# Kernel tuning notes

Hardware: AMD Instinct MI355X
Metric: run time of the kernel (lower is better)

Reference implementation:

```python
import jax, jax.numpy as jnp
import numpy as np

N_NODES = 20000
N_EDGES = 40000
N_GRAPHS = 500
D_IN = 32     # initial_dim_gcn
D_E = 16      # edge_dim_feature
H1 = 100      # hidden_dim_nn_1
H2 = 20       # hidden_dim_nn_2
F1 = 50       # hidden_dim_fcn_1


def setup_inputs() -> dict:
    key = jax.random.key(0)
    ks = jax.random.split(key, 16)
    s = lambda k, shp, fan: (jax.random.normal(k, shp, jnp.float32) / np.sqrt(fan)).astype(jnp.float32)
    return {
        "x": jax.random.normal(ks[0], (N_NODES, D_IN), jnp.float32),
        "edge_attr": jax.random.normal(ks[1], (N_EDGES, D_E), jnp.float32),
        "edge_index": jax.random.randint(ks[2], (2, N_EDGES), 0, N_NODES, jnp.int64),
        "batch": jnp.sort(jax.random.randint(ks[3], (N_NODES,), 0, N_GRAPHS, jnp.int64)),
        # NNConv layer 1: edge MLP Linear(D_E -> D_IN*H1), root weight, bias
        "nn1_W": s(ks[4], (D_E, D_IN * H1), D_E),
        "nn1_b": jnp.zeros((D_IN * H1,), jnp.float32),
        "root1": s(ks[5], (D_IN, H1), D_IN),
        "bias1": jnp.zeros((H1,), jnp.float32),
        # NNConv layer 2: edge MLP Linear(D_E -> H1*H2), root weight, bias
        "nn2_W": s(ks[6], (D_E, H1 * H2), D_E),
        "nn2_b": jnp.zeros((H1 * H2,), jnp.float32),
        "root2": s(ks[7], (H1, H2), H1),
        "bias2": jnp.zeros((H2,), jnp.float32),
        # FCN head
        "lin1_W": s(ks[8], (H2, F1), H2),
        "lin1_b": jnp.zeros((F1,), jnp.float32),
        "lin2_W": s(ks[9], (F1, 1), F1),
        "lin2_b": jnp.zeros((1,), jnp.float32),
    }


def _nnconv(x, src, dst, edge_attr, nnW, nnb, root, bias, d_in, d_out):
    # per-edge weight matrices: [E, d_in, d_out]
    theta = (edge_attr @ nnW + nnb).reshape(-1, d_in, d_out)
    # gather source features, per-edge matmul, scatter-add to targets
    msg = jnp.einsum('ei,eio->eo', x[src], theta)            # [E, d_out]
    agg = jax.ops.segment_sum(msg, dst, num_segments=x.shape[0])
    return agg + x @ root + bias


def reference(x, edge_attr, edge_index, batch,
              nn1_W, nn1_b, root1, bias1,
              nn2_W, nn2_b, root2, bias2,
              lin1_W, lin1_b, lin2_W, lin2_b):
    src, dst = edge_index[0], edge_index[1]  # PyG: message from j=src, aggregate at i=dst
    h = jax.nn.relu(_nnconv(x, src, dst, edge_attr, nn1_W, nn1_b, root1, bias1, D_IN, H1))
    h = jax.nn.relu(_nnconv(h, src, dst, edge_attr, nn2_W, nn2_b, root2, bias2, H1, H2))
    g = jax.ops.segment_sum(h, batch, num_segments=N_GRAPHS)  # sum-pool readout [G, H2]
    g = jax.nn.relu(g @ lin1_W + lin1_b)
    out = g @ lin2_W + lin2_b
    return out.reshape(-1)
```

## Files before the change

### kernel.cpp

```cpp
#include <hip/hip_runtime.h>
#include <hip/hip_fp16.h>

#define N_NODES 20000
#define N_EDGES 40000
#define N_GRAPHS 500
#define D_IN 32
#define D_E 16
#define H1 100
#define H2 20
#define F1 50

#define EB1 64
#define YNB 12
#define ET3 12

using h2f = __attribute__((ext_vector_type(2))) _Float16;
using h8f = __attribute__((ext_vector_type(8))) _Float16;
using f4  = __attribute__((ext_vector_type(4))) float;

__global__ __launch_bounds__(256) void prep_kernel(
    const float* __restrict__ nn1W, const float* __restrict__ nn1b,
    const float* __restrict__ nn2W, const float* __restrict__ nn2b,
    const float* __restrict__ root1, const float* __restrict__ bias1,
    const float* __restrict__ x,
    unsigned short* __restrict__ Wfrag1, unsigned short* __restrict__ Wfrag2,
    float* __restrict__ pre1, float* __restrict__ zbase)
{
  __shared__ float sroot1[D_IN * H1];
  __shared__ float sxl[YNB * D_IN];
  const int t   = threadIdx.x;
  const int tid = blockIdx.x * 256 + t;

  if (tid < 544 * 112) {
    const int c  = tid / 3584;
    const int r  = tid % 3584;
    const int to = r / 512;
    const int l  = (r % 512) >> 3;
    const int j  = r & 7;
    const int i  = (l >> 4) * 8 + j;
    const int o  = to * 16 + (l & 15);
    float v = 0.f;
    if (o < H1) v = (c < 16) ? nn1W[c * (D_IN * H1) + i * H1 + o] : nn1b[i * H1 + o];
    _Float16 hv = (_Float16)v;
    Wfrag1[tid] = __builtin_bit_cast(unsigned short, hv);
  } else if (tid < 544 * 112 + 17 * 4096) {
    const int t2 = tid - 544 * 112;
    const int c  = t2 >> 12;
    const int q  = (t2 >> 10) & 3;
    const int to = (t2 >> 9) & 1;
    const int l  = (t2 >> 3) & 63;
    const int j  = t2 & 7;
    const int i  = q * 32 + (l >> 4) * 8 + j;
    const int o  = to * 16 + (l & 15);
    float v = 0.f;
    if (i < H1 && o < H2)
      v = (c < 16) ? nn2W[c * (H1 * H2) + i * H2 + o] : nn2b[i * H2 + o];
    _Float16 hv = (_Float16)v;
    Wfrag2[t2] = __builtin_bit_cast(unsigned short, hv);
  }

  {
    float4* zp = (float4*)zbase;
    for (int i = tid; i < 102500; i += 512 * 256)
      zp[i] = make_float4(0.f, 0.f, 0.f, 0.f);
  }

  for (int idx = t; idx < 800; idx += 256)
    *(float4*)&sroot1[idx * 4] = *(const float4*)&root1[idx * 4];

  for (int tile = blockIdx.x; tile < 1667; tile += 512) {
    const int n0 = tile * YNB;
    __syncthreads();
    if (t < 96) {
      const int fo = t * 4;
      const int nn = fo >> 5;
      float4 v = make_float4(0.f, 0.f, 0.f, 0.f);
      if (n0 + nn < N_NODES) v = *(const float4*)&x[(size_t)n0 * D_IN + fo];
      *(float4*)&sxl[fo] = v;
    }
    __syncthreads();
    for (int idx = t; idx < YNB * H1; idx += 256) {
      const int nn = idx / H1, i = idx - nn * H1;
      const int n = n0 + nn;
      if (n < N_NODES) {
        float v = bias1[i];
        #pragma unroll 8
        for (int d = 0; d < D_IN; ++d)
          v = fmaf(sxl[nn * D_IN + d], sroot1[d * H1 + i], v);
        pre1[(size_t)n0 * H1 + idx] = v;
      }
    }
  }
}

__global__ __launch_bounds__(256, 3) void edge1_kernel(
    const float* __restrict__ x, const float* __restrict__ ea,
    const int* __restrict__ eidx, const unsigned short* __restrict__ Wfrag,
    float* __restrict__ agg1)
{
  __shared__ uint4 Plds[4 * 64];
  __shared__ uint4 Blds[2][7 * 64];
  __shared__ int   sdst[EB1];

  const int t    = threadIdx.x;
  const int lane = t & 63;
  const int w    = t >> 6;
  const int e0   = blockIdx.x * EB1;

  const int e_loc = t >> 2;
  const int jg    = t & 3;
  const int src   = eidx[e0 + e_loc];

  h2f xh[4];
  {
    const float4* xp = (const float4*)&x[(size_t)src * D_IN + jg * 8];
    float4 v0 = xp[0], v1 = xp[1];
    float xf[8] = {v0.x, v0.y, v0.z, v0.w, v1.x, v1.y, v1.z, v1.w};
    #pragma unroll
    for (int j = 0; j < 4; ++j) {
      h2f p; p[0] = (_Float16)xf[2*j]; p[1] = (_Float16)xf[2*j+1]; xh[j] = p;
    }
  }
  _Float16 eh[17];
  {
    const float4* ep = (const float4*)&ea[(size_t)(e0 + e_loc) * D_E];
    float4 v0 = ep[0], v1 = ep[1], v2 = ep[2], v3 = ep[3];
    float ef[16] = {v0.x,v0.y,v0.z,v0.w, v1.x,v1.y,v1.z,v1.w,
                    v2.x,v2.y,v2.z,v2.w, v3.x,v3.y,v3.z,v3.w};
    #pragma unroll
    for (int k = 0; k < 16; ++k) eh[k] = (_Float16)ef[k];
    eh[16] = (_Float16)1.0f;
  }
  if (t < EB1) sdst[t] = eidx[N_EDGES + e0 + t];

  const uint4* __restrict__ Bf = (const uint4*)Wfrag;
  {
    uint4 s0 = Bf[t];
    uint4 s1;
    if (t < 192) s1 = Bf[256 + t];
    Blds[0][t] = s0;
    if (t < 192) Blds[0][256 + t] = s1;
  }
  __syncthreads();

  f4 acc[7];
  #pragma unroll
  for (int to = 0; to < 7; ++to) acc[to] = f4{0.f, 0.f, 0.f, 0.f};

  const int pslot = w * 64 + (e_loc & 15) + 16 * jg;

  #pragma unroll
  for (int c = 0; c < 17; ++c) {
    uint4 s0, s1;
    if (c < 16) {
      const uint4* bn = Bf + (c + 1) * 448;
      s0 = bn[t];
      if (t < 192) s1 = bn[256 + t];
    }
    h2f es; es[0] = eh[c]; es[1] = eh[c];
    unsigned int pk[4];
    #pragma unroll
    for (int j = 0; j < 4; ++j) {
      h2f pr = xh[j] * es;
      pk[j] = __builtin_bit_cast(unsigned int, pr);
    }
    Plds[pslot] = make_uint4(pk[0], pk[1], pk[2], pk[3]);

    uint4 a = Plds[w * 64 + lane];
    h8f A = __builtin_bit_cast(h8f, a);

    const uint4* bb = &Blds[c & 1][0];
    #pragma unroll
    for (int to = 0; to < 7; ++to) {
      h8f B = __builtin_bit_cast(h8f, bb[to * 64 + lane]);
      acc[to] = __builtin_amdgcn_mfma_f32_16x16x32_f16(A, B, acc[to], 0, 0, 0);
    }
    if (c < 16) {
      Blds[(c + 1) & 1][t] = s0;
      if (t < 192) Blds[(c + 1) & 1][256 + t] = s1;
    }
    __syncthreads();
  }

  const int col = lane & 15, rowg = lane >> 4;
  #pragma unroll
  for (int r = 0; r < 4; ++r) {
    const int el = w * 16 + rowg * 4 + r;
    const int d = sdst[el];
    float* ap = agg1 + (size_t)d * H1;
    #pragma unroll
    for (int to = 0; to < 7; ++to) {
      const int o = to * 16 + col;
      if (o < H1) unsafeAtomicAdd(&ap[o], acc[to][r]);
    }
  }
}

__global__ __launch_bounds__(256, 3) void edge2m_kernel(
    const float* __restrict__ pre1, const float* __restrict__ ea,
    const int* __restrict__ eidx, const unsigned short* __restrict__ Wfrag2,
    float* __restrict__ agg2)
{
  __shared__ uint4 Plds[4][4][64];
  __shared__ uint4 Blds[2][512];
  __shared__ int   sdst[EB1];

  const int t    = threadIdx.x;
  const int lane = t & 63;
  const int w    = t >> 6;
  const int e0   = blockIdx.x * EB1;

  const int e_loc = t >> 2;
  const int jg    = t & 3;
  const int m     = e_loc & 15;
  const int src   = eidx[e0 + e_loc];

  h2f xh[16];
  {
    float xf[32];
    const float* hp = &pre1[(size_t)src * H1 + jg * 32];
    if (jg < 3) {
      #pragma unroll
      for (int q4 = 0; q4 < 8; ++q4) {
        float4 v = *(const float4*)&hp[q4 * 4];
        xf[q4*4+0] = fmaxf(v.x, 0.f); xf[q4*4+1] = fmaxf(v.y, 0.f);
        xf[q4*4+2] = fmaxf(v.z, 0.f); xf[q4*4+3] = fmaxf(v.w, 0.f);
      }
    } else {
      float4 v = *(const float4*)hp;
      xf[0] = fmaxf(v.x, 0.f); xf[1] = fmaxf(v.y, 0.f);
      xf[2] = fmaxf(v.z, 0.f); xf[3] = fmaxf(v.w, 0.f);
      #pragma unroll
      for (int ii = 4; ii < 32; ++ii) xf[ii] = 0.f;
    }
    #pragma unroll
    for (int j2 = 0; j2 < 16; ++j2) {
      h2f p; p[0] = (_Float16)xf[2*j2]; p[1] = (_Float16)xf[2*j2+1]; xh[j2] = p;
    }
  }
  _Float16 eh[17];
  {
    const float4* ep = (const float4*)&ea[(size_t)(e0 + e_loc) * D_E];
    float4 v0 = ep[0], v1 = ep[1], v2 = ep[2], v3 = ep[3];
    float ef[16] = {v0.x,v0.y,v0.z,v0.w, v1.x,v1.y,v1.z,v1.w,
                    v2.x,v2.y,v2.z,v2.w, v3.x,v3.y,v3.z,v3.w};
    #pragma unroll
    for (int k = 0; k < 16; ++k) eh[k] = (_Float16)ef[k];
    eh[16] = (_Float16)1.0f;
  }
  if (t < EB1) sdst[t] = eidx[N_EDGES + e0 + t];

  const uint4* __restrict__ Bf = (const uint4*)Wfrag2;
  {
    uint4 s0 = Bf[t];
    uint4 s1 = Bf[256 + t];
    Blds[0][t] = s0;
    Blds[0][256 + t] = s1;
  }
  {
    h2f es; es[0] = eh[0]; es[1] = eh[0];
    unsigned int pk[16];
    #pragma unroll
    for (int j2 = 0; j2 < 16; ++j2) {
      h2f pr = xh[j2] * es;
      pk[j2] = __builtin_bit_cast(unsigned int, pr);
    }
    #pragma unroll
    for (int oc = 0; oc < 4; ++oc)
      Plds[w][jg][16 * oc + m] = make_uint4(pk[4*oc], pk[4*oc+1], pk[4*oc+2], pk[4*oc+3]);
  }
  __syncthreads();

  f4 acc0 = f4{0.f, 0.f, 0.f, 0.f};
  f4 acc1 = f4{0.f, 0.f, 0.f, 0.f};

  #pragma unroll
  for (int c = 0; c < 17; ++c) {
    const int buf = c & 1;
    uint4 s0, s1;
    if (c < 16) {
      const uint4* bn = Bf + (c + 1) * 512;
      s0 = bn[t];
      s1 = bn[256 + t];
    }
    #pragma unroll
    for (int q = 0; q < 4; ++q) {
      uint4 a  = Plds[w][q][lane];
      uint4 b0 = Blds[buf][q * 128 + lane];
      uint4 b1 = Blds[buf][q * 128 + 64 + lane];
      h8f A  = __builtin_bit_cast(h8f, a);
      h8f B0 = __builtin_bit_cast(h8f, b0);
      h8f B1 = __builtin_bit_cast(h8f, b1);
      acc0 = __builtin_amdgcn_mfma_f32_16x16x32_f16(A, B0, acc0, 0, 0, 0);
      acc1 = __builtin_amdgcn_mfma_f32_16x16x32_f16(A, B1, acc1, 0, 0, 0);
    }
    if (c < 16) {
      h2f es; es[0] = eh[c + 1]; es[1] = eh[c + 1];
      unsigned int pk[16];
      #pragma unroll
      for (int j2 = 0; j2 < 16; ++j2) {
        h2f pr = xh[j2] * es;
        pk[j2] = __builtin_bit_cast(unsigned int, pr);
      }
      #pragma unroll
      for (int oc = 0; oc < 4; ++oc)
        Plds[w][jg][16 * oc + m] = make_uint4(pk[4*oc], pk[4*oc+1], pk[4*oc+2], pk[4*oc+3]);
      Blds[buf ^ 1][t] = s0;
      Blds[buf ^ 1][256 + t] = s1;
      __syncthreads();
    }
  }

  const int col = lane & 15, rowg = lane >> 4;
  #pragma unroll
  for (int r = 0; r < 4; ++r) {
    const int el = w * 16 + rowg * 4 + r;
    const int d  = sdst[el];
    float* ap = agg2 + (size_t)d * H2;
    unsafeAtomicAdd(&ap[col], acc0[r]);
    if (col < 4) unsafeAtomicAdd(&ap[16 + col], acc1[r]);
  }
}

__global__ __launch_bounds__(256) void node2_pool_kernel(
    const float* __restrict__ pre1, const float* __restrict__ agg2,
    const float* __restrict__ root2, const float* __restrict__ bias2,
    const int* __restrict__ batch, float* __restrict__ g)
{
  __shared__ float sroot[H1 * H2];
  __shared__ float sv[ET3][H2];
  __shared__ int   sg[ET3];
  const int t  = threadIdx.x;
  const int n0 = blockIdx.x * ET3;

  for (int idx = t; idx < (H1 * H2) / 4; idx += 256)
    *(float4*)&sroot[idx * 4] = *(const float4*)&root2[idx * 4];
  if (t < ET3) {
    const int n = n0 + t;
    sg[t] = (n < N_NODES) ? batch[n] : -1;
  }
  __syncthreads();

  const int nl = t / H2, o = t % H2;
  const int n = n0 + nl;
  if (nl < ET3) {
    float v = 0.f;
    if (n < N_NODES) {
      v = agg2[(size_t)n * H2 + o] + bias2[o];
      const float* hr = &pre1[(size_t)n * H1];
      #pragma unroll 5
      for (int i = 0; i < H1; i += 4) {
        const float4 hv = *(const float4*)&hr[i];
        v = fmaf(fmaxf(hv.x, 0.f), sroot[(i    ) * H2 + o], v);
        v = fmaf(fmaxf(hv.y, 0.f), sroot[(i + 1) * H2 + o], v);
        v = fmaf(fmaxf(hv.z, 0.f), sroot[(i + 2) * H2 + o], v);
        v = fmaf(fmaxf(hv.w, 0.f), sroot[(i + 3) * H2 + o], v);
      }
      v = fmaxf(v, 0.f);
    }
    sv[nl][o] = v;
  }
  __syncthreads();

  if (t < H2) {
    float run = 0.f;
    int cur = sg[0];
    #pragma unroll
    for (int r = 0; r < ET3; ++r) {
      const int gid = sg[r];
      if (gid != cur) {
        if (cur >= 0) unsafeAtomicAdd(&g[cur * H2 + t], run);
        run = 0.f; cur = gid;
      }
      run += sv[r][t];
    }
    if (cur >= 0) unsafeAtomicAdd(&g[cur * H2 + t], run);
  }
}

__global__ __launch_bounds__(64) void final_kernel(
    const float* __restrict__ g, const float* __restrict__ lin1W,
    const float* __restrict__ lin1b, const float* __restrict__ lin2W,
    const float* __restrict__ lin2b, float* __restrict__ out)
{
  const int gr = blockIdx.x;
  const int tt = threadIdx.x;
  float v = 0.f;
  if (tt < F1) {
    float s = lin1b[tt];
    #pragma unroll
    for (int o = 0; o < H2; ++o) s = fmaf(g[gr * H2 + o], lin1W[o * F1 + tt], s);
    v = fmaxf(s, 0.f) * lin2W[tt];
  }
  #pragma unroll
  for (int off = 32; off > 0; off >>= 1) v += __shfl_down(v, off, 64);
  if (tt == 0) out[gr] = v + lin2b[0];
}

extern "C" void kernel_launch(void* const* d_in, const int* in_sizes, int n_in,
                              void* d_out, int out_size, void* d_ws, size_t ws_size,
                              hipStream_t stream) {
  const float* x     = (const float*)d_in[0];
  const float* ea    = (const float*)d_in[1];
  const int*   eidx  = (const int*)d_in[2];
  const int*   batch = (const int*)d_in[3];
  const float* nn1W  = (const float*)d_in[4];
  const float* nn1b  = (const float*)d_in[5];
  const float* root1 = (const float*)d_in[6];
  const float* bias1 = (const float*)d_in[7];
  const float* nn2W  = (const float*)d_in[8];
  const float* nn2b  = (const float*)d_in[9];
  const float* root2 = (const float*)d_in[10];
  const float* bias2 = (const float*)d_in[11];
  const float* lin1W = (const float*)d_in[12];
  const float* lin1b = (const float*)d_in[13];
  const float* lin2W = (const float*)d_in[14];
  const float* lin2b = (const float*)d_in[15];
  float* out = (float*)d_out;

  float* ws   = (float*)d_ws;
  float* pre1 = ws;
  float* agg2 = pre1 + N_NODES * H1;
  float* g    = agg2 + N_NODES * H2;
  float* h1   = g    + N_GRAPHS * H2;
  unsigned short* Wfrag1 = (unsigned short*)(h1 + (size_t)N_NODES * H1);
  unsigned short* Wfrag2 = Wfrag1 + 61440;

  prep_kernel<<<512, 256, 0, stream>>>(nn1W, nn1b, nn2W, nn2b, root1, bias1, x,
                                       Wfrag1, Wfrag2, pre1, agg2);
  edge1_kernel<<<N_EDGES / EB1, 256, 0, stream>>>(x, ea, eidx, Wfrag1, pre1);
  edge2m_kernel<<<N_EDGES / EB1, 256, 0, stream>>>(pre1, ea, eidx, Wfrag2, agg2);
  node2_pool_kernel<<<(N_NODES + ET3 - 1) / ET3, 256, 0, stream>>>(
      pre1, agg2, root2, bias2, batch, g);
  final_kernel<<<N_GRAPHS, 64, 0, stream>>>(g, lin1W, lin1b, lin2W, lin2b, out);
}
```

Baseline: 174.5 us.

## Double edges per block in edge1 and fuse final MLP into pool kernel

edge1 now handles 128 edges per block. Each wave runs two MFMA edge tiles that share the same weight fragment loaded from LDS, which halves the weight-staging traffic per edge. Occupancy is lowered to 2 blocks per SM to fit the larger register footprint. The final FCN kernel is folded into the pooling kernel through a last-block-done atomic counter, removing one launch. The trade-offs are a serial tail in which one block computes all 500 graphs, and lower occupancy in edge1.

```diff
diff --git a/kernel.cpp b/kernel.cpp
--- a/kernel.cpp
+++ b/kernel.cpp
@@ -10,7 +10,8 @@
 #define H2 20
 #define F1 50
 
-#define EB1 64
+#define EB1 128
+#define EB2 64
 #define YNB 12
 #define ET3 12
 
@@ -61,7 +62,7 @@
 
   {
     float4* zp = (float4*)zbase;
-    for (int i = tid; i < 102500; i += 512 * 256)
+    for (int i = tid; i < 102501; i += 512 * 256)
       zp[i] = make_float4(0.f, 0.f, 0.f, 0.f);
   }
 
@@ -93,12 +94,12 @@
   }
 }
 
-__global__ __launch_bounds__(256, 3) void edge1_kernel(
+__global__ __launch_bounds__(256, 2) void edge1_kernel(
     const float* __restrict__ x, const float* __restrict__ ea,
     const int* __restrict__ eidx, const unsigned short* __restrict__ Wfrag,
-    float* __restrict__ agg1)
+    float* __restrict__ pre1)
 {
-  __shared__ uint4 Plds[4 * 64];
+  __shared__ uint4 Plds[8 * 64];
   __shared__ uint4 Blds[2][7 * 64];
   __shared__ int   sdst[EB1];
 
@@ -107,23 +108,25 @@
   const int w    = t >> 6;
   const int e0   = blockIdx.x * EB1;
 
-  const int e_loc = t >> 2;
-  const int jg    = t & 3;
-  const int src   = eidx[e0 + e_loc];
-
-  h2f xh[4];
-  {
-    const float4* xp = (const float4*)&x[(size_t)src * D_IN + jg * 8];
-    float4 v0 = xp[0], v1 = xp[1];
-    float xf[8] = {v0.x, v0.y, v0.z, v0.w, v1.x, v1.y, v1.z, v1.w};
-    #pragma unroll
-    for (int j = 0; j < 4; ++j) {
+  const int e_loc = t >> 1;
+  const int ih    = t & 1;
+  const int ec    = min(e0 + e_loc, N_EDGES - 1);
+  const int src   = eidx[ec];
+
+  h2f xh[8];
+  {
+    const float4* xp = (const float4*)&x[(size_t)src * D_IN + ih * 16];
+    float4 v0 = xp[0], v1 = xp[1], v2 = xp[2], v3 = xp[3];
+    float xf[16] = {v0.x,v0.y,v0.z,v0.w, v1.x,v1.y,v1.z,v1.w,
+                    v2.x,v2.y,v2.z,v2.w, v3.x,v3.y,v3.z,v3.w};
+    #pragma unroll
+    for (int j = 0; j < 8; ++j) {
       h2f p; p[0] = (_Float16)xf[2*j]; p[1] = (_Float16)xf[2*j+1]; xh[j] = p;
     }
   }
   _Float16 eh[17];
   {
-    const float4* ep = (const float4*)&ea[(size_t)(e0 + e_loc) * D_E];
+    const float4* ep = (const float4*)&ea[(size_t)ec * D_E];
     float4 v0 = ep[0], v1 = ep[1], v2 = ep[2], v3 = ep[3];
     float ef[16] = {v0.x,v0.y,v0.z,v0.w, v1.x,v1.y,v1.z,v1.w,
                     v2.x,v2.y,v2.z,v2.w, v3.x,v3.y,v3.z,v3.w};
@@ -131,9 +134,10 @@
     for (int k = 0; k < 16; ++k) eh[k] = (_Float16)ef[k];
     eh[16] = (_Float16)1.0f;
   }
-  if (t < EB1) sdst[t] = eidx[N_EDGES + e0 + t];
+  if (t < EB1) sdst[t] = eidx[N_EDGES + min(e0 + t, N_EDGES - 1)];
 
   const uint4* __restrict__ Bf = (const uint4*)Wfrag;
+
   {
     uint4 s0 = Bf[t];
     uint4 s1;
@@ -143,11 +147,15 @@
   }
   __syncthreads();
 
-  f4 acc[7];
+  f4 acc[2][7];
   #pragma unroll
-  for (int to = 0; to < 7; ++to) acc[to] = f4{0.f, 0.f, 0.f, 0.f};
-
-  const int pslot = w * 64 + (e_loc & 15) + 16 * jg;
+  for (int te = 0; te < 2; ++te)
+    #pragma unroll
+    for (int to = 0; to < 7; ++to)
+      acc[te][to] = f4{0.f, 0.f, 0.f, 0.f};
+
+  const int etw   = 2 * w;
+  const int pbase = (e_loc >> 4) * 64 + (e_loc & 15) + 16 * (2 * ih);
 
   #pragma unroll
   for (int c = 0; c < 17; ++c) {
@@ -157,24 +165,30 @@
       s0 = bn[t];
       if (t < 192) s1 = bn[256 + t];
     }
+
     h2f es; es[0] = eh[c]; es[1] = eh[c];
-    unsigned int pk[4];
-    #pragma unroll
-    for (int j = 0; j < 4; ++j) {
+    unsigned int pk[8];
+    #pragma unroll
+    for (int j = 0; j < 8; ++j) {
       h2f pr = xh[j] * es;
       pk[j] = __builtin_bit_cast(unsigned int, pr);
     }
-    Plds[pslot] = make_uint4(pk[0], pk[1], pk[2], pk[3]);
-
-    uint4 a = Plds[w * 64 + lane];
-    h8f A = __builtin_bit_cast(h8f, a);
+    Plds[pbase]      = make_uint4(pk[0], pk[1], pk[2], pk[3]);
+    Plds[pbase + 16] = make_uint4(pk[4], pk[5], pk[6], pk[7]);
+
+    uint4 a0 = Plds[ etw      * 64 + lane];
+    uint4 a1 = Plds[(etw + 1) * 64 + lane];
+    h8f A0 = __builtin_bit_cast(h8f, a0);
+    h8f A1 = __builtin_bit_cast(h8f, a1);
 
     const uint4* bb = &Blds[c & 1][0];
     #pragma unroll
     for (int to = 0; to < 7; ++to) {
       h8f B = __builtin_bit_cast(h8f, bb[to * 64 + lane]);
-      acc[to] = __builtin_amdgcn_mfma_f32_16x16x32_f16(A, B, acc[to], 0, 0, 0);
-    }
+      acc[0][to] = __builtin_amdgcn_mfma_f32_16x16x32_f16(A0, B, acc[0][to], 0, 0, 0);
+      acc[1][to] = __builtin_amdgcn_mfma_f32_16x16x32_f16(A1, B, acc[1][to], 0, 0, 0);
+    }
+
     if (c < 16) {
       Blds[(c + 1) & 1][t] = s0;
       if (t < 192) Blds[(c + 1) & 1][256 + t] = s1;
@@ -184,14 +198,19 @@
 
   const int col = lane & 15, rowg = lane >> 4;
   #pragma unroll
-  for (int r = 0; r < 4; ++r) {
-    const int el = w * 16 + rowg * 4 + r;
-    const int d = sdst[el];
-    float* ap = agg1 + (size_t)d * H1;
-    #pragma unroll
-    for (int to = 0; to < 7; ++to) {
-      const int o = to * 16 + col;
-      if (o < H1) unsafeAtomicAdd(&ap[o], acc[to][r]);
+  for (int te = 0; te < 2; ++te) {
+    #pragma unroll
+    for (int r = 0; r < 4; ++r) {
+      const int el = (etw + te) * 16 + rowg * 4 + r;
+      if (e0 + el < N_EDGES) {
+        const int d = sdst[el];
+        float* ap = pre1 + (size_t)d * H1;
+        #pragma unroll
+        for (int to = 0; to < 7; ++to) {
+          const int o = to * 16 + col;
+          if (o < H1) unsafeAtomicAdd(&ap[o], acc[te][to][r]);
+        }
+      }
     }
   }
 }
@@ -203,12 +222,12 @@
 {
   __shared__ uint4 Plds[4][4][64];
   __shared__ uint4 Blds[2][512];
-  __shared__ int   sdst[EB1];
+  __shared__ int   sdst[EB2];
 
   const int t    = threadIdx.x;
   const int lane = t & 63;
   const int w    = t >> 6;
-  const int e0   = blockIdx.x * EB1;
+  const int e0   = blockIdx.x * EB2;
 
   const int e_loc = t >> 2;
   const int jg    = t & 3;
@@ -248,7 +267,7 @@
     for (int k = 0; k < 16; ++k) eh[k] = (_Float16)ef[k];
     eh[16] = (_Float16)1.0f;
   }
-  if (t < EB1) sdst[t] = eidx[N_EDGES + e0 + t];
+  if (t < EB2) sdst[t] = eidx[N_EDGES + e0 + t];
 
   const uint4* __restrict__ Bf = (const uint4*)Wfrag2;
   {
@@ -322,14 +341,19 @@
   }
 }
 
-__global__ __launch_bounds__(256) void node2_pool_kernel(
+__global__ __launch_bounds__(256) void node2_pool_final_kernel(
     const float* __restrict__ pre1, const float* __restrict__ agg2,
     const float* __restrict__ root2, const float* __restrict__ bias2,
-    const int* __restrict__ batch, float* __restrict__ g)
+    const int* __restrict__ batch, float* __restrict__ g,
+    int* __restrict__ cnt,
+    const float* __restrict__ lin1W, const float* __restrict__ lin1b,
+    const float* __restrict__ lin2W, const float* __restrict__ lin2b,
+    float* __restrict__ out)
 {
   __shared__ float sroot[H1 * H2];
   __shared__ float sv[ET3][H2];
   __shared__ int   sg[ET3];
+  __shared__ int   lastFlag;
   const int t  = threadIdx.x;
   const int n0 = blockIdx.x * ET3;
 
@@ -376,25 +400,31 @@
     }
     if (cur >= 0) unsafeAtomicAdd(&g[cur * H2 + t], run);
   }
-}
-
-__global__ __launch_bounds__(64) void final_kernel(
-    const float* __restrict__ g, const float* __restrict__ lin1W,
-    const float* __restrict__ lin1b, const float* __restrict__ lin2W,
-    const float* __restrict__ lin2b, float* __restrict__ out)
-{
-  const int gr = blockIdx.x;
-  const int tt = threadIdx.x;
-  float v = 0.f;
-  if (tt < F1) {
-    float s = lin1b[tt];
-    #pragma unroll
-    for (int o = 0; o < H2; ++o) s = fmaf(g[gr * H2 + o], lin1W[o * F1 + tt], s);
-    v = fmaxf(s, 0.f) * lin2W[tt];
-  }
-  #pragma unroll
-  for (int off = 32; off > 0; off >>= 1) v += __shfl_down(v, off, 64);
-  if (tt == 0) out[gr] = v + lin2b[0];
+
+  __threadfence();
+  if (t == 0) {
+    int prev = atomicAdd(cnt, 1);
+    lastFlag = (prev == (int)gridDim.x - 1);
+  }
+  __syncthreads();
+  if (lastFlag) {
+    __threadfence();
+    for (int gr = t; gr < N_GRAPHS; gr += 256) {
+      float gv[H2];
+      #pragma unroll
+      for (int oo = 0; oo < H2; ++oo)
+        gv[oo] = unsafeAtomicAdd(&g[gr * H2 + oo], 0.f);
+      float acc = 0.f;
+      for (int f = 0; f < F1; ++f) {
+        float s = lin1b[f];
+        #pragma unroll
+        for (int oo = 0; oo < H2; ++oo)
+          s = fmaf(gv[oo], lin1W[oo * F1 + f], s);
+        acc = fmaf(fmaxf(s, 0.f), lin2W[f], acc);
+      }
+      out[gr] = acc + lin2b[0];
+    }
+  }
 }
 
 extern "C" void kernel_launch(void* const* d_in, const int* in_sizes, int n_in,
@@ -422,15 +452,16 @@
   float* pre1 = ws;
   float* agg2 = pre1 + N_NODES * H1;
   float* g    = agg2 + N_NODES * H2;
-  float* h1   = g    + N_GRAPHS * H2;
+  int*   cnt  = (int*)(g + N_GRAPHS * H2);
+  float* h1   = g + N_GRAPHS * H2 + 4;
   unsigned short* Wfrag1 = (unsigned short*)(h1 + (size_t)N_NODES * H1);
   unsigned short* Wfrag2 = Wfrag1 + 61440;
 
   prep_kernel<<<512, 256, 0, stream>>>(nn1W, nn1b, nn2W, nn2b, root1, bias1, x,
                                        Wfrag1, Wfrag2, pre1, agg2);
-  edge1_kernel<<<N_EDGES / EB1, 256, 0, stream>>>(x, ea, eidx, Wfrag1, pre1);
-  edge2m_kernel<<<N_EDGES / EB1, 256, 0, stream>>>(pre1, ea, eidx, Wfrag2, agg2);
-  node2_pool_kernel<<<(N_NODES + ET3 - 1) / ET3, 256, 0, stream>>>(
-      pre1, agg2, root2, bias2, batch, g);
-  final_kernel<<<N_GRAPHS, 64, 0, stream>>>(g, lin1W, lin1b, lin2W, lin2b, out);
+  edge1_kernel<<<(N_EDGES + EB1 - 1) / EB1, 256, 0, stream>>>(
+      x, ea, eidx, Wfrag1, pre1);
+  edge2m_kernel<<<N_EDGES / EB2, 256, 0, stream>>>(pre1, ea, eidx, Wfrag2, agg2);
+  node2_pool_final_kernel<<<(N_NODES + ET3 - 1) / ET3, 256, 0, stream>>>(
+      pre1, agg2, root2, bias2, batch, g, cnt, lin1W, lin1b, lin2W, lin2b, out);
 }
```

Result: slower. 298.6 us (+71.1%).
